# Performance work log

Hardware: AMD Instinct MI355X
Metric: run time of the kernel (lower is better)

## Reference

```python
import jax, jax.numpy as jnp
import numpy as np

T, M, N = 16, 1024, 10000
N_IN, N_B = 8000, 100


def setup_inputs() -> dict:
    key = jax.random.key(0)
    ks = jax.random.split(key, 7)
    x = jax.random.normal(ks[0], (T, 3, M), dtype=jnp.float32)
    weight = jax.random.normal(ks[1], (N, 4 * M, 2), dtype=jnp.float32) * 0.02
    # 1-based node indices, as the original module subtracts 1
    node_in = jax.random.randint(ks[2], (N_IN,), 1, N + 1)
    top = jax.random.randint(ks[3], (N_B,), 1, N + 1)
    bottom = jax.random.randint(ks[4], (N_B,), 1, N + 1)
    left = jax.random.randint(ks[5], (N_B,), 1, N + 1)
    right = jax.random.randint(ks[6], (N_B,), 1, N + 1)
    return {"x": x, "weight": weight, "node_in": node_in,
            "top": top, "bottom": bottom, "left": left, "right": right}


def reference(x, weight, node_in, top, bottom, left, right):
    t, _, m = x.shape
    # Vectorized form of the nested scatter loop:
    # x_out[i, 4m:4m+4] = [x[i,0,m], x[i,2,m], x[i,2,m], x[i,1,m]]
    x_out = jnp.stack([x[:, 0, :], x[:, 2, :], x[:, 2, :], x[:, 1, :]],
                      axis=-1).reshape(t, 4 * m)  # [T, 4M]
    # torch.matmul([1,T,4M], [N,4M,2]) broadcast -> [N, T, 2]
    f = jnp.einsum('ti,nio->nto', x_out, weight)
    f_in = f[node_in - 1]  # [N_in, T, 2]
    s_top = f[top - 1, :, 1].sum(axis=0)      # [T]
    s_bot = f[bottom - 1, :, 1].sum(axis=0)
    s_left = f[left - 1, :, 0].sum(axis=0)
    s_right = f[right - 1, :, 0].sum(axis=0)
    f_b = jnp.stack([s_top, s_bot, s_left, s_right,
                     s_top + s_bot, s_left + s_right], axis=0)[..., None]  # [6, T, 1]
    return f_in, f_b
```

## Files before the change

### kernel.cpp

```cpp
#include <hip/hip_runtime.h>
#include <stdint.h>

#define T_DIM 16
#define M_DIM 1024
#define N_NODES 10000
#define NB 100
#define N_IN 8000
#define KI 4096
#define KP 8192
#define CHUNKS 16
#define I_CHUNK (KI / CHUNKS)
#define M_CHUNK (I_CHUNK / 4)
#define STEPS ((KP / CHUNKS) / 32)
#define PITCH (I_CHUNK + 4)
#define TILES 625
#define SLAB (N_NODES * T_DIM * 2)

typedef short short8 __attribute__((ext_vector_type(8)));
typedef float f32x4 __attribute__((ext_vector_type(4)));

__device__ __forceinline__ unsigned int fbits(float f) {
    return __builtin_bit_cast(unsigned int, f);
}
__device__ __forceinline__ unsigned int bf16rne(unsigned int u) {
    return (u + 0x7FFFu + ((u >> 16) & 1u)) >> 16;
}
__device__ __forceinline__ unsigned int pack2bf(float a, float b) {
    return bf16rne(fbits(a)) | (bf16rne(fbits(b)) << 16);
}
__device__ __forceinline__ unsigned int cvtpk(float a, float b) {
    unsigned int r;
    asm("v_cvt_pk_bf16_f32 %0, %1, %2" : "=v"(r) : "v"(a), "v"(b));
    return r;
}

__global__ __launch_bounds__(1024) void dedup_kernel(
    const int* __restrict__ node_in,
    const int* __restrict__ top, const int* __restrict__ bottom,
    const int* __restrict__ left, const int* __restrict__ right,
    int* __restrict__ counter, int* __restrict__ list)
{
    __shared__ int flags[N_NODES];
    __shared__ int lcnt;
    const int tid = threadIdx.x;
    for (int i = tid; i < N_NODES; i += 1024) flags[i] = 0;
    if (tid == 0) lcnt = 0;
    __syncthreads();
    for (int i = tid; i < N_IN + 4 * NB; i += 1024) {
        int v;
        if (i < N_IN)              v = node_in[i];
        else if (i < N_IN + NB)    v = top[i - N_IN];
        else if (i < N_IN + 2*NB)  v = bottom[i - N_IN - NB];
        else if (i < N_IN + 3*NB)  v = left[i - N_IN - 2*NB];
        else                       v = right[i - N_IN - 3*NB];
        flags[v - 1] = 1;
    }
    __syncthreads();
    const int lane = tid & 63;
    for (int i = tid; i < N_NODES; i += 1024) {
        int f = flags[i];
        unsigned long long mask = __ballot(f);
        int prefix = __popcll(mask & ((1ull << lane) - 1ull));
        int base = 0;
        if (lane == 0) base = atomicAdd(&lcnt, (int)__popcll(mask));
        base = __shfl(base, 0);
        if (f) list[base + prefix] = i;
    }
    __syncthreads();
    if (tid == 0) *counter = lcnt;
}

__global__ __launch_bounds__(256) void gemm_kernel(
    const float* __restrict__ x,
    const float* __restrict__ weight,
    const int* __restrict__ list,
    const int* __restrict__ counter,
    float* __restrict__ fws)
{
    __shared__ unsigned short lds_x[T_DIM * PITCH];

    const int tid = threadIdx.x;
    const int chunk = blockIdx.y;

    const int cnt = *counter;
    if (blockIdx.x * 64 >= cnt) return;

    for (int q = tid; q < T_DIM * M_CHUNK; q += 256) {
        int t = q >> 6;
        int mloc = q & 63;
        int m = chunk * M_CHUNK + mloc;
        const float* xb = x + t * 3 * M_DIM + m;
        float v0 = xb[0];
        float v1 = xb[M_DIM];
        float v2 = xb[2 * M_DIM];
        unsigned int w0 = cvtpk(v0, v2);
        unsigned int w1 = cvtpk(v2, v1);
        *(uint2*)&lds_x[t * PITCH + mloc * 4] = make_uint2(w0, w1);
    }
    __syncthreads();

    const int wave = tid >> 6;
    const int lane = tid & 63;
    const int tile = blockIdx.x * 4 + wave;
    if (tile * 16 >= cnt) return;

    const int col = lane & 15;
    const int quad = lane >> 4;
    const int idx = tile * 16 + col;
    const int n = (idx < cnt) ? list[idx] : 0;

    const float* wp =
        weight + (size_t)n * KP + (size_t)chunk * (KP / CHUNKS) + quad * 8;
    const unsigned short* xrow = &lds_x[(lane & 15) * PITCH + quad * 4];

    f32x4 acc0 = {0.f, 0.f, 0.f, 0.f};
    f32x4 acc1 = {0.f, 0.f, 0.f, 0.f};

#define GSTEP(S, LO, HI) do {                                               \
        union { unsigned int ui[4]; short8 v; } Bu;                         \
        Bu.ui[0] = cvtpk((LO).x, (LO).y);                                   \
        Bu.ui[1] = cvtpk((LO).z, (LO).w);                                   \
        Bu.ui[2] = cvtpk((HI).x, (HI).y);                                   \
        Bu.ui[3] = cvtpk((HI).z, (HI).w);                                   \
        uint2 u = *(const uint2*)(xrow + (S) * 16);                         \
        union { unsigned int ui[4]; short8 v; } A0u, A1u;                   \
        A0u.ui[0] = u.x & 0xFFFFu;      A0u.ui[1] = u.x >> 16;              \
        A0u.ui[2] = u.y & 0xFFFFu;      A0u.ui[3] = u.y >> 16;              \
        A1u.ui[0] = u.x << 16;          A1u.ui[1] = u.x & 0xFFFF0000u;      \
        A1u.ui[2] = u.y << 16;          A1u.ui[3] = u.y & 0xFFFF0000u;      \
        acc0 = __builtin_amdgcn_mfma_f32_16x16x32_bf16(A0u.v, Bu.v, acc0, 0, 0, 0); \
        acc1 = __builtin_amdgcn_mfma_f32_16x16x32_bf16(A1u.v, Bu.v, acc1, 0, 0, 0); \
    } while (0)

    float4 p0l = *(const float4*)(wp + 0 * 32), p0h = *(const float4*)(wp + 0 * 32 + 4);
    float4 p1l = *(const float4*)(wp + 1 * 32), p1h = *(const float4*)(wp + 1 * 32 + 4);
    float4 p2l = *(const float4*)(wp + 2 * 32), p2h = *(const float4*)(wp + 2 * 32 + 4);
    float4 p3l = *(const float4*)(wp + 3 * 32), p3h = *(const float4*)(wp + 3 * 32 + 4);

    #pragma unroll 2
    for (int s = 0; s < STEPS; s += 4) {
        float4 lo, hi;
        lo = p0l; hi = p0h;
        if (s + 4 < STEPS) {
            p0l = *(const float4*)(wp + (s + 4) * 32);
            p0h = *(const float4*)(wp + (s + 4) * 32 + 4);
        }
        GSTEP(s + 0, lo, hi);
        lo = p1l; hi = p1h;
        if (s + 5 < STEPS) {
            p1l = *(const float4*)(wp + (s + 5) * 32);
            p1h = *(const float4*)(wp + (s + 5) * 32 + 4);
        }
        GSTEP(s + 1, lo, hi);
        lo = p2l; hi = p2h;
        if (s + 6 < STEPS) {
            p2l = *(const float4*)(wp + (s + 6) * 32);
            p2h = *(const float4*)(wp + (s + 6) * 32 + 4);
        }
        GSTEP(s + 2, lo, hi);
        lo = p3l; hi = p3h;
        if (s + 7 < STEPS) {
            p3l = *(const float4*)(wp + (s + 7) * 32);
            p3h = *(const float4*)(wp + (s + 7) * 32 + 4);
        }
        GSTEP(s + 3, lo, hi);
    }
#undef GSTEP

    float* slab = fws + (size_t)chunk * SLAB;
    #pragma unroll
    for (int r = 0; r < 4; ++r) {
        int t = quad * 4 + r;
        *(float2*)&slab[((size_t)n * T_DIM + t) * 2] = make_float2(acc0[r], acc1[r]);
    }
}

__global__ __launch_bounds__(256) void gather_kernel(
    const float* __restrict__ fws,
    const int* __restrict__ node_in,
    const int* __restrict__ top, const int* __restrict__ bottom,
    const int* __restrict__ left, const int* __restrict__ right,
    float* __restrict__ out)
{
    const int tid = threadIdx.x;
    if (blockIdx.x < 250) {
        int e4 = blockIdx.x * 1024 + tid * 4;
        int j = e4 >> 5;
        int rem = e4 & 31;
        size_t base = (size_t)(node_in[j] - 1) * 32 + rem;
        float4 v = {0.f, 0.f, 0.f, 0.f};
        #pragma unroll
        for (int c = 0; c < CHUNKS; ++c) {
            float4 s = *(const float4*)&fws[c * (size_t)SLAB + base];
            v.x += s.x; v.y += s.y; v.z += s.z; v.w += s.w;
        }
        *(float4*)&out[e4] = v;
    } else {
        __shared__ float red[256];
        __shared__ float sums[64];
        const int l = tid >> 6;
        const int t = (tid >> 2) & 15;
        const int p = tid & 3;
        const int* lp = (l == 0) ? top : (l == 1) ? bottom : (l == 2) ? left : right;
        const int osel = (l < 2) ? 1 : 0;
        float s = 0.f;
        for (int idx = p; idx < NB; idx += 4) {
            size_t base = (size_t)(lp[idx] - 1) * 32 + t * 2 + osel;
            #pragma unroll
            for (int c = 0; c < CHUNKS; ++c) s += fws[c * (size_t)SLAB + base];
        }
        red[tid] = s;
        __syncthreads();
        if (p == 0)
            sums[tid >> 2] = red[tid] + red[tid + 1] + red[tid + 2] + red[tid + 3];
        __syncthreads();
        if (tid < 96) {
            int row = tid >> 4;
            int tt = tid & 15;
            float v;
            if (row < 4)       v = sums[row * 16 + tt];
            else if (row == 4) v = sums[0 * 16 + tt] + sums[1 * 16 + tt];
            else               v = sums[2 * 16 + tt] + sums[3 * 16 + tt];
            out[256000 + tid] = v;
        }
    }
}

extern "C" void kernel_launch(void* const* d_in, const int* in_sizes, int n_in,
                              void* d_out, int out_size, void* d_ws, size_t ws_size,
                              hipStream_t stream)
{
    const float* x      = (const float*)d_in[0];
    const float* weight = (const float*)d_in[1];
    const int* node_in = (const int*)d_in[2];
    const int* top     = (const int*)d_in[3];
    const int* bottom  = (const int*)d_in[4];
    const int* left    = (const int*)d_in[5];
    const int* right   = (const int*)d_in[6];

    float* fws  = (float*)d_ws;
    int*   cnt  = (int*)(fws + (size_t)CHUNKS * SLAB);
    int*   list = cnt + 1;
    float* out  = (float*)d_out;

    dedup_kernel<<<1, 1024, 0, stream>>>(node_in, top, bottom, left, right, cnt, list);

    dim3 grid((TILES + 3) / 4, CHUNKS);
    gemm_kernel<<<grid, 256, 0, stream>>>(x, weight, list, cnt, fws);
    gather_kernel<<<251, 256, 0, stream>>>(fws, node_in, top, bottom, left, right, out);
}
```

Before: 463.2 us.

## Stage weight rows through LDS with coalesced per-node loads before MFMA

```diff
diff --git a/kernel.cpp b/kernel.cpp
--- a/kernel.cpp
+++ b/kernel.cpp
@@ -78,6 +78,7 @@
     float* __restrict__ fws)
 {
     __shared__ unsigned short lds_x[T_DIM * PITCH];
+    __shared__ unsigned short lds_b[4][16 * 256];
 
     const int tid = threadIdx.x;
     const int chunk = blockIdx.y;
@@ -109,63 +110,41 @@
     const int idx = tile * 16 + col;
     const int n = (idx < cnt) ? list[idx] : 0;
 
-    const float* wp =
-        weight + (size_t)n * KP + (size_t)chunk * (KP / CHUNKS) + quad * 8;
+    const size_t koff = (size_t)chunk * (KP / CHUNKS);
     const unsigned short* xrow = &lds_x[(lane & 15) * PITCH + quad * 4];
+    unsigned short* bb = lds_b[wave];
 
     f32x4 acc0 = {0.f, 0.f, 0.f, 0.f};
     f32x4 acc1 = {0.f, 0.f, 0.f, 0.f};
 
-#define GSTEP(S, LO, HI) do {                                               \
-        union { unsigned int ui[4]; short8 v; } Bu;                         \
-        Bu.ui[0] = cvtpk((LO).x, (LO).y);                                   \
-        Bu.ui[1] = cvtpk((LO).z, (LO).w);                                   \
-        Bu.ui[2] = cvtpk((HI).x, (HI).y);                                   \
-        Bu.ui[3] = cvtpk((HI).z, (HI).w);                                   \
-        uint2 u = *(const uint2*)(xrow + (S) * 16);                         \
-        union { unsigned int ui[4]; short8 v; } A0u, A1u;                   \
-        A0u.ui[0] = u.x & 0xFFFFu;      A0u.ui[1] = u.x >> 16;              \
-        A0u.ui[2] = u.y & 0xFFFFu;      A0u.ui[3] = u.y >> 16;              \
-        A1u.ui[0] = u.x << 16;          A1u.ui[1] = u.x & 0xFFFF0000u;      \
-        A1u.ui[2] = u.y << 16;          A1u.ui[3] = u.y & 0xFFFF0000u;      \
-        acc0 = __builtin_amdgcn_mfma_f32_16x16x32_bf16(A0u.v, Bu.v, acc0, 0, 0, 0); \
-        acc1 = __builtin_amdgcn_mfma_f32_16x16x32_bf16(A1u.v, Bu.v, acc1, 0, 0, 0); \
-    } while (0)
-
-    float4 p0l = *(const float4*)(wp + 0 * 32), p0h = *(const float4*)(wp + 0 * 32 + 4);
-    float4 p1l = *(const float4*)(wp + 1 * 32), p1h = *(const float4*)(wp + 1 * 32 + 4);
-    float4 p2l = *(const float4*)(wp + 2 * 32), p2h = *(const float4*)(wp + 2 * 32 + 4);
-    float4 p3l = *(const float4*)(wp + 3 * 32), p3h = *(const float4*)(wp + 3 * 32 + 4);
-
-    #pragma unroll 2
-    for (int s = 0; s < STEPS; s += 4) {
-        float4 lo, hi;
-        lo = p0l; hi = p0h;
-        if (s + 4 < STEPS) {
-            p0l = *(const float4*)(wp + (s + 4) * 32);
-            p0h = *(const float4*)(wp + (s + 4) * 32 + 4);
-        }
-        GSTEP(s + 0, lo, hi);
-        lo = p1l; hi = p1h;
-        if (s + 5 < STEPS) {
-            p1l = *(const float4*)(wp + (s + 5) * 32);
-            p1h = *(const float4*)(wp + (s + 5) * 32 + 4);
-        }
-        GSTEP(s + 1, lo, hi);
-        lo = p2l; hi = p2h;
-        if (s + 6 < STEPS) {
-            p2l = *(const float4*)(wp + (s + 6) * 32);
-            p2h = *(const float4*)(wp + (s + 6) * 32 + 4);
-        }
-        GSTEP(s + 2, lo, hi);
-        lo = p3l; hi = p3h;
-        if (s + 7 < STEPS) {
-            p3l = *(const float4*)(wp + (s + 7) * 32);
-            p3h = *(const float4*)(wp + (s + 7) * 32 + 4);
-        }
-        GSTEP(s + 3, lo, hi);
-    }
-#undef GSTEP
+    #pragma unroll
+    for (int s = 0; s < 2; ++s) {
+        #pragma unroll
+        for (int nd = 0; nd < 16; ++nd) {
+            int nn = __shfl(n, nd);
+            const float* src = weight + (size_t)nn * KP + koff + s * 256 + lane * 4;
+            f32x4 w4 = *(const f32x4*)src;
+            unsigned int u0 = cvtpk(w4[0], w4[1]);
+            unsigned int u1 = cvtpk(w4[2], w4[3]);
+            *(uint2*)&bb[nd * 256 + lane * 4] = make_uint2(u0, u1);
+        }
+
+        #pragma unroll
+        for (int gs = 0; gs < 8; ++gs) {
+            short8 Bv = *(const short8*)&bb[col * 256 + gs * 32 + quad * 8];
+
+            int S = s * 8 + gs;
+            uint2 u = *(const uint2*)(xrow + S * 16);
+            union { unsigned int ui[4]; short8 v; } A0u, A1u;
+            A0u.ui[0] = u.x & 0xFFFFu;      A0u.ui[1] = u.x >> 16;
+            A0u.ui[2] = u.y & 0xFFFFu;      A0u.ui[3] = u.y >> 16;
+            A1u.ui[0] = u.x << 16;          A1u.ui[1] = u.x & 0xFFFF0000u;
+            A1u.ui[2] = u.y << 16;          A1u.ui[3] = u.y & 0xFFFF0000u;
+
+            acc0 = __builtin_amdgcn_mfma_f32_16x16x32_bf16(A0u.v, Bv, acc0, 0, 0, 0);
+            acc1 = __builtin_amdgcn_mfma_f32_16x16x32_bf16(A1u.v, Bv, acc1, 0, 0, 0);
+        }
+    }
 
     float* slab = fws + (size_t)chunk * SLAB;
     #pragma unroll
```

Result: no change. 461.4 us (-0.4%).
